# Performance work log

Hardware: AMD Instinct MI355X
Metric: run time of the kernel (lower is better)

## Reference

```python
import jax, jax.numpy as jnp
import numpy as np

D_MODEL = 1024
NHEAD = 16
HEAD_DIM = D_MODEL // NHEAD
EPS_NORM = 1e-6
EPS_RMS = 1e-6


def setup_inputs() -> dict:
    key = jax.random.key(0)
    ks = jax.random.split(key, 8)
    B, S = 2, 1024
    scale = 1.0 / np.sqrt(D_MODEL)
    x = jax.random.normal(ks[0], (B, S, D_MODEL), dtype=jnp.float32)
    Wq = jax.random.normal(ks[1], (D_MODEL, D_MODEL), dtype=jnp.float32) * scale
    Wk = jax.random.normal(ks[2], (D_MODEL, D_MODEL), dtype=jnp.float32) * scale
    Wv = jax.random.normal(ks[3], (D_MODEL, D_MODEL), dtype=jnp.float32) * scale
    Wb = jax.random.normal(ks[4], (NHEAD, D_MODEL), dtype=jnp.float32) * scale
    Wo = jax.random.normal(ks[5], (D_MODEL, D_MODEL), dtype=jnp.float32) * scale
    rms_w = jnp.ones((D_MODEL,), dtype=jnp.float32)
    return {"x": x, "Wq": Wq, "Wk": Wk, "Wv": Wv, "Wb": Wb, "Wo": Wo, "rms_w": rms_w}


def _l2_normalize(t):
    return t / (jnp.linalg.norm(t, axis=-1, keepdims=True) + EPS_NORM)


def _delta_forward(x, Wq, Wk, Wv, Wb, Wo, rms_w):
    B, S, dm = x.shape
    H, D = NHEAD, HEAD_DIM
    q = _l2_normalize(jax.nn.silu(x @ Wq.T).reshape(B, S, H, D))
    k = _l2_normalize(jax.nn.silu(x @ Wk.T).reshape(B, S, H, D))
    v = jax.nn.silu(x @ Wv.T).reshape(B, S, H, D)
    beta = jax.nn.sigmoid(x @ Wb.T) * 2.0  # (B,S,H), allow_neg_eigval doubles

    # time-major for scan: (S,B,H,D) / (S,B,H)
    qT = q.transpose(1, 0, 2, 3)
    kT = k.transpose(1, 0, 2, 3)
    vT = v.transpose(1, 0, 2, 3)
    bT = beta.transpose(1, 0, 2)

    def step(M, inp):
        qt, kt, vt, bt = inp
        # read state BEFORE update (strictly causal)
        out_t = jnp.einsum('bnh,bnhd->bnd', qt, M)
        retrieved = jnp.einsum('bnhd,bnd->bnh', M, kt)
        delta = vt - retrieved
        M = M + bt[..., None, None] * jnp.einsum('bnh,bnd->bnhd', kt, delta)
        return M, out_t

    M0 = jnp.zeros((B, H, D, D), dtype=x.dtype)
    _, outs = jax.lax.scan(step, M0, (qT, kT, vT, bT))  # (S,B,H,D)
    out = outs.transpose(1, 0, 2, 3).reshape(B, S, dm)

    # RMSNorm
    rms = jnp.sqrt(jnp.mean(out * out, axis=-1, keepdims=True) + EPS_RMS)
    out = out / rms * rms_w
    # output projection (dropout is identity in eval)
    return out @ Wo.T


def reference(x, Wq, Wk, Wv, Wb, Wo, rms_w):
    return _delta_forward(x, Wq, Wk, Wv, Wb, Wo, rms_w)
```

## Files before the change

kernel.cpp:

```cpp
#include <hip/hip_runtime.h>
#include <math.h>

#define D_MODEL 1024
#define NHEAD 16
#define HEAD_DIM 64
#define BATCH 2
#define SEQ 1024
#define ROWS (BATCH * SEQ)
#define RD (ROWS * D_MODEL)
#define WSZ (D_MODEL * D_MODEL)
#define CHUNK 64
#define NCHUNK (SEQ / CHUNK)

typedef __attribute__((ext_vector_type(8))) short bf16x8;
typedef __attribute__((ext_vector_type(8))) _Float16 f16x8;
typedef __attribute__((ext_vector_type(8))) unsigned short ushort8;
typedef __attribute__((ext_vector_type(4))) unsigned short us4;
typedef __attribute__((ext_vector_type(4))) float f32x4;
typedef __attribute__((ext_vector_type(4))) unsigned int uint4v;
typedef unsigned short ushort;

__device__ __forceinline__ void load_lds_16u(const unsigned short* g, unsigned short* l) {
    __builtin_amdgcn_global_load_lds((const __attribute__((address_space(1))) void*)g,
                                     (__attribute__((address_space(3))) void*)l, 16, 0, 0);
}
__device__ __forceinline__ unsigned short f2bf(float x) {
    unsigned int u = __float_as_uint(x);
    unsigned int r = (u + 0x7FFFu + ((u >> 16) & 1u)) >> 16;
    return (unsigned short)r;
}
__device__ __forceinline__ float bf2f(unsigned short h) {
    return __uint_as_float(((unsigned int)h) << 16);
}
__device__ __forceinline__ unsigned short f2h(float x) {
    _Float16 h = (_Float16)x;
    return __builtin_bit_cast(unsigned short, h);
}
__device__ __forceinline__ float lane_bcast(float v, int lane) {
    return __uint_as_float(__builtin_amdgcn_readlane(__float_as_uint(v), lane));
}
#define SUBST 512
#define FBUF (8 * SUBST * 2)
__device__ __forceinline__ int fidx(int r, int k) {
    return ((r >> 4) * 2 + (k >> 5)) * SUBST + ((((k & 31) >> 3) << 4) + (r & 15)) * 8 + (k & 7);
}


__global__ __launch_bounds__(256) void split_kernel(const float* __restrict__ X,
                                                    unsigned short* __restrict__ H,
                                                    int n4) {
    int i = blockIdx.x * 256 + threadIdx.x;
    if (i >= n4) return;
    float4 v = ((const float4*)X)[i];
    us4 h;
    h.x = f2h(v.x); h.y = f2h(v.y); h.z = f2h(v.z); h.w = f2h(v.w);
    ((us4*)H)[i] = h;
}

__global__ __launch_bounds__(256) void split3_kernel(const float* __restrict__ W0,
                                                     const float* __restrict__ W1,
                                                     const float* __restrict__ W2,
                                                     unsigned short* __restrict__ H0,
                                                     unsigned short* __restrict__ H1,
                                                     unsigned short* __restrict__ H2) {
    const int n4 = WSZ / 4;
    int i = blockIdx.x * 256 + threadIdx.x;
    const int which = i / n4;
    const int j = i - which * n4;
    const float* X = (which == 0) ? W0 : (which == 1) ? W1 : W2;
    unsigned short* H = (which == 0) ? H0 : (which == 1) ? H1 : H2;
    float4 v = ((const float4*)X)[j];
    us4 h;
    h.x = f2h(v.x); h.y = f2h(v.y); h.z = f2h(v.z); h.w = f2h(v.w);
    ((us4*)H)[j] = h;
}

template <int ACT>
__device__ __forceinline__ void gemm_core_f16(const unsigned short* __restrict__ Ah,
                                              const unsigned short* __restrict__ Bh,
                                              float* __restrict__ C,
                                              int M, int N, int K,
                                              unsigned short* LA0, unsigned short* LB0) {
    const int t = threadIdx.x;
    const int wave = t >> 6, lane = t & 63;
    const int wm = wave >> 1, wn = wave & 1;
    const int m16 = lane & 15, kg = lane >> 4;
    const int row0 = blockIdx.y * 128, col0 = blockIdx.x * 64;

    f32x4 acc[4][2];
#pragma unroll
    for (int i = 0; i < 4; ++i)
#pragma unroll
        for (int j = 0; j < 2; ++j) acc[i][j] = (f32x4){0.f, 0.f, 0.f, 0.f};

    for (int k0 = 0; k0 < K; k0 += 32) {
#pragma unroll
        for (int ci = 0; ci < 3; ++ci) {
            const int c = wave * 3 + ci;
            const unsigned short* src;
            unsigned short* dst;
            int g16, rbase;
            if (c < 8) { src = Ah; dst = &LA0[c * 512];       g16 = c;     rbase = row0; }
            else       { src = Bh; dst = &LB0[(c - 8) * 512]; g16 = c - 8; rbase = col0; }
            const unsigned short* gp = src + (size_t)(rbase + g16 * 16 + m16) * K + k0 + kg * 8;
            load_lds_16u(gp, dst);
        }
        __syncthreads();

        f16x8 fah[4], fbh[2];
#pragma unroll
        for (int mt = 0; mt < 4; ++mt)
            fah[mt] = *(const f16x8*)&LA0[(wm * 4 + mt) * 512 + lane * 8];
#pragma unroll
        for (int nt = 0; nt < 2; ++nt)
            fbh[nt] = *(const f16x8*)&LB0[(wn * 2 + nt) * 512 + lane * 8];
#pragma unroll
        for (int mt = 0; mt < 4; ++mt)
#pragma unroll
            for (int nt = 0; nt < 2; ++nt)
                acc[mt][nt] = __builtin_amdgcn_mfma_f32_16x16x32_f16(fah[mt], fbh[nt], acc[mt][nt], 0, 0, 0);
        __syncthreads();
    }

#pragma unroll
    for (int mt = 0; mt < 4; ++mt)
#pragma unroll
        for (int nt = 0; nt < 2; ++nt) {
            const int rowb = row0 + wm * 64 + mt * 16 + kg * 4;
            const int col  = col0 + wn * 32 + nt * 16 + m16;
#pragma unroll
            for (int rg = 0; rg < 4; ++rg) {
                float v = acc[mt][nt][rg];
                if (ACT == 1) v = v / (1.f + expf(-v));
                C[(size_t)(rowb + rg) * N + col] = v;
            }
        }
}

template <int ACT>
__global__ __launch_bounds__(256) void gemm_f16s(const unsigned short* __restrict__ Ah,
                                                 const unsigned short* __restrict__ Bh,
                                                 float* __restrict__ C,
                                                 int M, int N, int K) {
    __shared__ unsigned short LA[8 * 512];
    __shared__ unsigned short LB[4 * 512];
    gemm_core_f16<ACT>(Ah, Bh, C, M, N, K, LA, LB);
}

__global__ __launch_bounds__(256) void gemm_qkv(const unsigned short* __restrict__ Ah,
                                                const unsigned short* __restrict__ Bqh,
                                                const unsigned short* __restrict__ Bkh,
                                                const unsigned short* __restrict__ Bvh,
                                                float* __restrict__ Cq,
                                                float* __restrict__ Ck,
                                                float* __restrict__ Cv) {
    __shared__ unsigned short LA[8 * 512];
    __shared__ unsigned short LB[4 * 512];
    const int z = blockIdx.z;
    const unsigned short* Bh = (z == 0) ? Bqh : (z == 1) ? Bkh : Bvh;
    float* C = (z == 0) ? Cq : (z == 1) ? Ck : Cv;
    gemm_core_f16<1>(Ah, Bh, C, ROWS, D_MODEL, D_MODEL, LA, LB);
}

#define LDST 40
template <int ACT>
__global__ __launch_bounds__(256) void gemm_mfma(const float* __restrict__ A,
                                                 const float* __restrict__ B,
                                                 float* __restrict__ C,
                                                 int M, int N, int K) {
    __shared__ unsigned short Ahi[128 * LDST], Alo[128 * LDST];
    __shared__ unsigned short Bhi[128 * LDST], Blo[128 * LDST];

    const int t = threadIdx.x;
    const int wave = t >> 6, lane = t & 63;
    const int wm = wave >> 1, wn = wave & 1;
    const int row0 = blockIdx.y * 128, col0 = blockIdx.x * 128;
    const int sr = t >> 1;
    const int sh = t & 1;
    const int m16 = lane & 15, kg = lane >> 4;

    f32x4 acc[4][4];
#pragma unroll
    for (int i = 0; i < 4; ++i)
#pragma unroll
        for (int j = 0; j < 4; ++j) acc[i][j] = (f32x4){0.f, 0.f, 0.f, 0.f};

    const float* ga = A + (size_t)(row0 + sr) * K + sh * 16;
    const float* gb = B + (size_t)(col0 + sr) * K + sh * 16;
    const int sbase = sr * LDST + sh * 16;

    for (int k0 = 0; k0 < K; k0 += 32) {
        float af[16], bf[16];
#pragma unroll
        for (int i = 0; i < 4; ++i) {
            float4 a4 = *(const float4*)(ga + k0 + i * 4);
            float4 b4 = *(const float4*)(gb + k0 + i * 4);
            af[i * 4 + 0] = a4.x; af[i * 4 + 1] = a4.y; af[i * 4 + 2] = a4.z; af[i * 4 + 3] = a4.w;
            bf[i * 4 + 0] = b4.x; bf[i * 4 + 1] = b4.y; bf[i * 4 + 2] = b4.z; bf[i * 4 + 3] = b4.w;
        }
        ushort8 ah0, ah1, al0, al1, bh0, bh1, bl0, bl1;
#pragma unroll
        for (int j = 0; j < 8; ++j) {
            unsigned short h = f2bf(af[j]);       ah0[j] = h; al0[j] = f2bf(af[j] - bf2f(h));
            h = f2bf(af[j + 8]);                  ah1[j] = h; al1[j] = f2bf(af[j + 8] - bf2f(h));
            h = f2bf(bf[j]);                      bh0[j] = h; bl0[j] = f2bf(bf[j] - bf2f(h));
            h = f2bf(bf[j + 8]);                  bh1[j] = h; bl1[j] = f2bf(bf[j + 8] - bf2f(h));
        }
        *(ushort8*)&Ahi[sbase] = ah0;  *(ushort8*)&Ahi[sbase + 8] = ah1;
        *(ushort8*)&Alo[sbase] = al0;  *(ushort8*)&Alo[sbase + 8] = al1;
        *(ushort8*)&Bhi[sbase] = bh0;  *(ushort8*)&Bhi[sbase + 8] = bh1;
        *(ushort8*)&Blo[sbase] = bl0;  *(ushort8*)&Blo[sbase + 8] = bl1;
        __syncthreads();

        bf16x8 fah[4], fal[4], fbh[4], fbl[4];
#pragma unroll
        for (int i = 0; i < 4; ++i) {
            const int ar = (wm * 64 + i * 16 + m16) * LDST + kg * 8;
            const int br = (wn * 64 + i * 16 + m16) * LDST + kg * 8;
            fah[i] = *(const bf16x8*)&Ahi[ar];
            fal[i] = *(const bf16x8*)&Alo[ar];
            fbh[i] = *(const bf16x8*)&Bhi[br];
            fbl[i] = *(const bf16x8*)&Blo[br];
        }
#pragma unroll
        for (int i = 0; i < 4; ++i)
#pragma unroll
            for (int j = 0; j < 4; ++j) {
                acc[i][j] = __builtin_amdgcn_mfma_f32_16x16x32_bf16(fal[i], fbh[j], acc[i][j], 0, 0, 0);
                acc[i][j] = __builtin_amdgcn_mfma_f32_16x16x32_bf16(fah[i], fbl[j], acc[i][j], 0, 0, 0);
                acc[i][j] = __builtin_amdgcn_mfma_f32_16x16x32_bf16(fah[i], fbh[j], acc[i][j], 0, 0, 0);
            }
        __syncthreads();
    }

#pragma unroll
    for (int i = 0; i < 4; ++i)
#pragma unroll
        for (int j = 0; j < 4; ++j) {
            const int col = col0 + wn * 64 + j * 16 + m16;
            const int rowb = row0 + wm * 64 + i * 16 + kg * 4;
#pragma unroll
            for (int rg = 0; rg < 4; ++rg) {
                float v = acc[i][j][rg];
                if (ACT == 1) v = v / (1.f + expf(-v));
                C[(size_t)(rowb + rg) * N + col] = v;
            }
        }
}

__global__ __launch_bounds__(256) void beta_kernel(const float* __restrict__ x,
                                                   const float* __restrict__ Wb,
                                                   float* __restrict__ beta) {
    const int wave = blockIdx.x * 4 + (threadIdx.x >> 6);
    const int lane = threadIdx.x & 63;
    const float* xr = x + (size_t)wave * D_MODEL;
    float xv[16];
#pragma unroll
    for (int j = 0; j < 16; ++j) xv[j] = xr[lane + 64 * j];
    for (int n = 0; n < NHEAD; ++n) {
        const float* wr = Wb + (size_t)n * D_MODEL;
        float s = 0.f;
#pragma unroll
        for (int j = 0; j < 16; ++j) s += xv[j] * wr[lane + 64 * j];
#pragma unroll
        for (int off = 32; off; off >>= 1) s += __shfl_xor(s, off);
        if (lane == 0) beta[(size_t)wave * NHEAD + n] = 2.f / (1.f + expf(-s));
    }
}

__global__ __launch_bounds__(256) void norm_qk(float* __restrict__ Q,
                                               float* __restrict__ Kp) {
    const int TOT = ROWS * NHEAD;
    int wave = blockIdx.x * 4 + (threadIdx.x >> 6);
    const int lane = threadIdx.x & 63;
    float* T = (wave < TOT) ? Q : Kp;
    int w = (wave < TOT) ? wave : wave - TOT;
    float* p = T + (size_t)(w >> 4) * D_MODEL + (size_t)(w & 15) * HEAD_DIM;
    float v = p[lane];
    float ss = v * v;
#pragma unroll
    for (int off = 32; off; off >>= 1) ss += __shfl_xor(ss, off);
    p[lane] = v / (sqrtf(ss) + 1e-6f);
}

#define SMEM_SCAN 156160

__global__ __launch_bounds__(512, 1) void scan_chunked(const float* __restrict__ Qg,
                                                       const float* __restrict__ Kg,
                                                       const float* __restrict__ Vg,
                                                       const float* __restrict__ Btg,
                                                       float* __restrict__ Yg) {
    extern __shared__ char smem[];
    ushort* Mh_  = (ushort*)(smem + 0 * FBUF);
    ushort* Ml_  = (ushort*)(smem + 1 * FBUF);
    ushort* MTh_ = (ushort*)(smem + 2 * FBUF);
    ushort* MTl_ = (ushort*)(smem + 3 * FBUF);
    ushort* KTh_ = (ushort*)(smem + 4 * FBUF);
    ushort* KTl_ = (ushort*)(smem + 5 * FBUF);
    ushort* V0h_ = (ushort*)(smem + 6 * FBUF);
    ushort* V0l_ = (ushort*)(smem + 7 * FBUF);
    ushort* Wh_  = V0h_;
    ushort* Wl_  = V0l_;
    ushort* Gh_  = (ushort*)(smem + 8 * FBUF);
    ushort* Gl_  = (ushort*)(smem + 9 * FBUF);
    ushort* Kh_  = (ushort*)(smem + 10 * FBUF);
    ushort* Kl_  = (ushort*)(smem + 11 * FBUF);
    ushort* DTh_ = Kh_;
    ushort* DTl_ = Kl_;
    ushort* Qh_  = (ushort*)(smem + 12 * FBUF);
    ushort* Ql_  = (ushort*)(smem + 13 * FBUF);
    float*  C032 = (float*)(smem + 14 * FBUF);
    ushort* Ah_  = (ushort*)(smem + 14 * FBUF + 16640);
    ushort* Al_  = (ushort*)(smem + 15 * FBUF + 16640);
    float*  N32  = (float*)(smem + 16 * FBUF + 16640);
    float*  bAll = (float*)(smem + 16 * FBUF + 16640 + 4352);

    const int b = blockIdx.x >> 4;
    const int n = blockIdx.x & 15;
    const int t = threadIdx.x;
    const int wave = t >> 6, lane = t & 63;
    const int wm = wave >> 1, wn = wave & 1;
    const int m16 = lane & 15, kg = lane >> 4;
    const int bS = b * SEQ;
    const int nOff = n * HEAD_DIM;
    const int r = t >> 3, g = t & 7;

    f32x4 Macc[2];
    Macc[0] = (f32x4){0.f, 0.f, 0.f, 0.f};
    Macc[1] = (f32x4){0.f, 0.f, 0.f, 0.f};

    auto load_af = [&](const ushort* Xh, const ushort* Xl, int tm, bf16x8* oh, bf16x8* ol) {
        const int lo8 = lane * 8;
#pragma unroll
        for (int half = 0; half < 2; ++half) {
            oh[half] = *(const bf16x8*)&Xh[(tm * 2 + half) * SUBST + lo8];
            ol[half] = *(const bf16x8*)&Xl[(tm * 2 + half) * SUBST + lo8];
        }
    };
    auto prod_cA = [&](const bf16x8* ah, const bf16x8* al,
                       const ushort* Bh, const ushort* Bl, int tn, f32x4* acc) {
        const int lo8 = lane * 8;
#pragma unroll
        for (int half = 0; half < 2; ++half) {
#pragma unroll
            for (int j = 0; j < 2; ++j) {
                const int jg = tn * 2 + j;
                bf16x8 bh = *(const bf16x8*)&Bh[(jg * 2 + half) * SUBST + lo8];
                bf16x8 bl = *(const bf16x8*)&Bl[(jg * 2 + half) * SUBST + lo8];
                acc[j] = __builtin_amdgcn_mfma_f32_16x16x32_bf16(al[half], bh, acc[j], 0, 0, 0);
                acc[j] = __builtin_amdgcn_mfma_f32_16x16x32_bf16(ah[half], bl, acc[j], 0, 0, 0);
                acc[j] = __builtin_amdgcn_mfma_f32_16x16x32_bf16(ah[half], bh, acc[j], 0, 0, 0);
            }
        }
    };

    for (int i = t; i < SEQ; i += 512) bAll[i] = Btg[(size_t)(bS + i) * NHEAD + n];

    float4 pk0, pk1, pq0, pq1;
    float pv[8];
    auto issue_pf = [&](int cc) {
        const int so = cc * CHUNK;
        const float* gK = Kg + (size_t)(bS + so + r) * D_MODEL + nOff + g * 8;
        const float* gQ = Qg + (size_t)(bS + so + r) * D_MODEL + nOff + g * 8;
        pk0 = ((const float4*)gK)[0]; pk1 = ((const float4*)gK)[1];
        pq0 = ((const float4*)gQ)[0]; pq1 = ((const float4*)gQ)[1];
        const float* gV = Vg + (size_t)(bS + so) * D_MODEL + nOff;
#pragma unroll
        for (int j = 0; j < 2; ++j)
#pragma unroll
            for (int rg = 0; rg < 4; ++rg)
                pv[j * 4 + rg] = gV[(size_t)(wm * 16 + kg * 4 + rg) * D_MODEL + wn * 32 + j * 16 + m16];
    };
    issue_pf(0);

    for (int c = 0; c < NCHUNK; ++c) {
        const int s0 = c * CHUNK;

        {
            float kf[8] = {pk0.x, pk0.y, pk0.z, pk0.w, pk1.x, pk1.y, pk1.z, pk1.w};
            float qf[8] = {pq0.x, pq0.y, pq0.z, pq0.w, pq1.x, pq1.y, pq1.z, pq1.w};
            ushort8 kh8, kl8, qh8, ql8;
            ushort khv[8], klv[8];
#pragma unroll
            for (int e = 0; e < 8; ++e) {
                ushort h = f2bf(kf[e]);
                ushort l = f2bf(kf[e] - bf2f(h));
                khv[e] = h; klv[e] = l;
                kh8[e] = h; kl8[e] = l;
                h = f2bf(qf[e]); l = f2bf(qf[e] - bf2f(h));
                qh8[e] = h; ql8[e] = l;
            }
            const int o0 = fidx(r, g * 8);
            *(ushort8*)&Kh_[o0] = kh8;
            *(ushort8*)&Kl_[o0] = kl8;
            *(ushort8*)&Qh_[o0] = qh8;
            *(ushort8*)&Ql_[o0] = ql8;
#pragma unroll
            for (int e = 0; e < 8; ++e) {
                const int ib = fidx(g * 8 + e, r);
                KTh_[ib] = khv[e]; KTl_[ib] = klv[e];
            }
        }
        __syncthreads();

        bf16x8 kah[2], kal[2];
        f32x4 V0acc[2];
        {
            load_af(Kh_, Kl_, wm, kah, kal);
            V0acc[0] = (f32x4){0.f, 0.f, 0.f, 0.f};
            V0acc[1] = (f32x4){0.f, 0.f, 0.f, 0.f};
            if (c > 0) prod_cA(kah, kal, Mh_, Ml_, wn, V0acc);
#pragma unroll
            for (int j = 0; j < 2; ++j)
#pragma unroll
                for (int rg = 0; rg < 4; ++rg)
                    V0acc[j][rg] = pv[j * 4 + rg] - V0acc[j][rg];
#pragma unroll
            for (int j = 0; j < 2; ++j)
#pragma unroll
                for (int rg = 0; rg < 4; ++rg) {
                    const int row = wm * 16 + kg * 4 + rg, col = wn * 32 + j * 16 + m16;
                    const float v0 = V0acc[j][rg];
                    const ushort h = f2bf(v0);
                    const int ii = fidx(row, col);
                    V0h_[ii] = h; V0l_[ii] = f2bf(v0 - bf2f(h));
                }
            f32x4 aacc[2];
            aacc[0] = (f32x4){0.f, 0.f, 0.f, 0.f};
            aacc[1] = (f32x4){0.f, 0.f, 0.f, 0.f};
            prod_cA(kah, kal, Kh_, Kl_, wn, aacc);
#pragma unroll
            for (int j = 0; j < 2; ++j)
#pragma unroll
                for (int rg = 0; rg < 4; ++rg) {
                    const int row = wm * 16 + kg * 4 + rg, col = wn * 32 + j * 16 + m16;
                    const float av = aacc[j][rg];
                    const ushort h = f2bf(av);
                    const int ii = fidx(row, col);
                    Ah_[ii] = h; Al_[ii] = f2bf(av - bf2f(h));
                }
        }
        __syncthreads();

        {
            f32x4 cacc[2];
            cacc[0] = (f32x4){0.f, 0.f, 0.f, 0.f};
            cacc[1] = (f32x4){0.f, 0.f, 0.f, 0.f};
            prod_cA(kah, kal, V0h_, V0l_, wn, cacc);
#pragma unroll
            for (int j = 0; j < 2; ++j)
#pragma unroll
                for (int rg = 0; rg < 4; ++rg) {
                    const int row = wm * 16 + kg * 4 + rg, col = wn * 32 + j * 16 + m16;
                    C032[row * 65 + col] = cacc[j][rg];
                }
        }
        __syncthreads();

        if (c + 1 < NCHUNK) issue_pf(c + 1);

        f32x4 yacc[2][2];

        if (wave == 0) {
#pragma unroll
            for (int i0 = 0; i0 < 16; ++i0)
                ((uint4v*)Wh_)[i0 * 64 + lane] = (uint4v){0u, 0u, 0u, 0u};

#pragma unroll
            for (int J = 0; J < 4; ++J) {
                float Nreg[16];
                if (J > 0) {
                    const int lo8 = lane * 8;
#pragma unroll
                    for (int band = 0; band < 4; ++band) {
                        f32x4 acc1 = (f32x4){0.f, 0.f, 0.f, 0.f};
#pragma unroll
                        for (int half = 0; half < 2; ++half) {
                            bf16x8 ah = *(const bf16x8*)&Ah_[(band * 2 + half) * SUBST + lo8];
                            bf16x8 al = *(const bf16x8*)&Al_[(band * 2 + half) * SUBST + lo8];
                            bf16x8 bh = *(const bf16x8*)&Wh_[(J * 2 + half) * SUBST + lo8];
                            bf16x8 bl = *(const bf16x8*)&Wl_[(J * 2 + half) * SUBST + lo8];
                            acc1 = __builtin_amdgcn_mfma_f32_16x16x32_bf16(al, bh, acc1, 0, 0, 0);
                            acc1 = __builtin_amdgcn_mfma_f32_16x16x32_bf16(ah, bl, acc1, 0, 0, 0);
                            acc1 = __builtin_amdgcn_mfma_f32_16x16x32_bf16(ah, bh, acc1, 0, 0, 0);
                        }
#pragma unroll
                        for (int rg = 0; rg < 4; ++rg)
                            N32[(band * 16 + kg * 4 + rg) * 17 + m16] = acc1[rg];
                    }
#pragma unroll
                    for (int j = 0; j < 16; ++j) Nreg[j] = N32[lane * 17 + j];
                }

                float Areg[16], CNreg[16];
                {
                    bf16x8 a0 = *(const bf16x8*)&Ah_[fidx(lane, 16 * J)];
                    bf16x8 a1 = *(const bf16x8*)&Ah_[fidx(lane, 16 * J + 8)];
                    bf16x8 b0 = *(const bf16x8*)&Al_[fidx(lane, 16 * J)];
                    bf16x8 b1 = *(const bf16x8*)&Al_[fidx(lane, 16 * J + 8)];
#pragma unroll
                    for (int e = 0; e < 8; ++e) {
                        Areg[e]     = bf2f((ushort)a0[e]) + bf2f((ushort)b0[e]);
                        Areg[e + 8] = bf2f((ushort)a1[e]) + bf2f((ushort)b1[e]);
                    }
#pragma unroll
                    for (int j = 0; j < 16; ++j) CNreg[j] = C032[lane * 65 + 16 * J + j];
                    if (J > 0) {
#pragma unroll
                        for (int j = 0; j < 16; ++j) CNreg[j] += Nreg[j];
                    }
                }
                float bvreg = bAll[s0 + 16 * J + m16];

                float wreg[16];
#pragma unroll
                for (int j = 0; j < 16; ++j) {
                    float sA = CNreg[j], sB = 0.f;
#pragma unroll
                    for (int jj = 0; jj < 16; ++jj) {
                        if (jj < j) {
                            float pr = Areg[jj] * lane_bcast(wreg[jj], 16 * J + j);
                            if (jj & 1) sB += pr; else sA += pr;
                        }
                    }
                    float sum = sA + sB;
                    float beta_s = lane_bcast(bvreg, j);
                    wreg[j] = (lane > 16 * J + j) ? (-beta_s * sum) : 0.f;
                }

                {
                    ushort8 h8[2], l8[2];
#pragma unroll
                    for (int e = 0; e < 16; ++e) {
                        ushort h = f2bf(wreg[e]);
                        h8[e >> 3][e & 7] = h;
                        l8[e >> 3][e & 7] = f2bf(wreg[e] - bf2f(h));
                    }
                    const int o0 = fidx(lane, 16 * J), o1 = fidx(lane, 16 * J + 8);
                    *(ushort8*)&Wh_[o0] = h8[0]; *(ushort8*)&Wh_[o1] = h8[1];
                    *(ushort8*)&Wl_[o0] = l8[0]; *(ushort8*)&Wl_[o1] = l8[1];
                }
            }
        } else {
            const int nt_w = (wave == 4) ? 0 : ((wave <= 2) ? 2 : 1);
            const int wi = (wave < 4) ? (wave - 1) : (wave - 2);
#pragma unroll
            for (int ti = 0; ti < 2; ++ti) {
                if (ti >= nt_w) continue;
                const int T = (ti == 0) ? wi : (wi + 6);
                const int twm = T >> 1, twn = T & 1;
                bf16x8 qh2[2], ql2[2];
                load_af(Qh_, Ql_, twm, qh2, ql2);
                yacc[ti][0] = (f32x4){0.f, 0.f, 0.f, 0.f};
                yacc[ti][1] = (f32x4){0.f, 0.f, 0.f, 0.f};
                if (c > 0) prod_cA(qh2, ql2, MTh_, MTl_, twn, yacc[ti]);
                const bool gz = (twm * 16 + 15) <= (twn * 32);
                f32x4 ga[2];
                ga[0] = (f32x4){0.f, 0.f, 0.f, 0.f};
                ga[1] = (f32x4){0.f, 0.f, 0.f, 0.f};
                if (!gz) prod_cA(qh2, ql2, Kh_, Kl_, twn, ga);
#pragma unroll
                for (int j = 0; j < 2; ++j)
#pragma unroll
                    for (int rg = 0; rg < 4; ++rg) {
                        const int row = twm * 16 + kg * 4 + rg, col = twn * 32 + j * 16 + m16;
                        const float gv = (row > col) ? ga[j][rg] : 0.f;
                        const ushort h = f2bf(gv);
                        const int ii = fidx(row, col);
                        Gh_[ii] = h; Gl_[ii] = f2bf(gv - bf2f(h));
                    }
            }
        }
        __syncthreads();

        {
            f32x4 dacc[2];
            dacc[0] = V0acc[0]; dacc[1] = V0acc[1];
            bf16x8 wh2[2], wl2[2];
            load_af(Wh_, Wl_, wm, wh2, wl2);
            prod_cA(wh2, wl2, KTh_, KTl_, wn, dacc);
#pragma unroll
            for (int j = 0; j < 2; ++j)
#pragma unroll
                for (int rg = 0; rg < 4; ++rg) {
                    const int row = wm * 16 + kg * 4 + rg, col = wn * 32 + j * 16 + m16;
                    const float dv = dacc[j][rg] * bAll[s0 + row];
                    const ushort h = f2bf(dv);
                    const int ii = fidx(col, row);
                    DTh_[ii] = h; DTl_[ii] = f2bf(dv - bf2f(h));
                }
        }
        __syncthreads();

        if (wave != 0) {
            const int nt_w = (wave == 4) ? 0 : ((wave <= 2) ? 2 : 1);
            const int wi = (wave < 4) ? (wave - 1) : (wave - 2);
#pragma unroll
            for (int ti = 0; ti < 2; ++ti) {
                if (ti >= nt_w) continue;
                const int T = (ti == 0) ? wi : (wi + 6);
                const int twm = T >> 1, twn = T & 1;
                bf16x8 gh2[2], gl2[2];
                load_af(Gh_, Gl_, twm, gh2, gl2);
                prod_cA(gh2, gl2, DTh_, DTl_, twn, yacc[ti]);
#pragma unroll
                for (int j = 0; j < 2; ++j)
#pragma unroll
                    for (int rg = 0; rg < 4; ++rg) {
                        const int row = twm * 16 + kg * 4 + rg, col = twn * 32 + j * 16 + m16;
                        Yg[(size_t)(bS + s0 + row) * D_MODEL + nOff + col] = yacc[ti][j][rg];
                    }
            }
        }
        {
            bf16x8 kth[2], ktl[2];
            load_af(KTh_, KTl_, wm, kth, ktl);
            prod_cA(kth, ktl, DTh_, DTl_, wn, Macc);
            if (c < NCHUNK - 1) {
#pragma unroll
                for (int j = 0; j < 2; ++j)
#pragma unroll
                    for (int rg = 0; rg < 4; ++rg) {
                        const int row = wm * 16 + kg * 4 + rg, col = wn * 32 + j * 16 + m16;
                        const float mv = Macc[j][rg];
                        const ushort h = f2bf(mv), l = f2bf(mv - bf2f(h));
                        const int ii = fidx(row, col);
                        Mh_[ii] = h; Ml_[ii] = l;
                        const int iT = fidx(col, row);
                        MTh_[iT] = h; MTl_[iT] = l;
                    }
            }
        }
        __syncthreads();
    }
}

template <int SPLIT>
__global__ __launch_bounds__(256) void rmsnorm_kernel(float* __restrict__ Y,
                                                      const float* __restrict__ w,
                                                      unsigned short* __restrict__ H) {
    __shared__ float red[4];
    float* y = Y + (size_t)blockIdx.x * D_MODEL;
    const int t = threadIdx.x;
    const int wv = t >> 6, ln = t & 63;
    float4 v = ((float4*)y)[t];
    float ss = v.x * v.x + v.y * v.y + v.z * v.z + v.w * v.w;
#pragma unroll
    for (int off = 32; off; off >>= 1) ss += __shfl_xor(ss, off);
    if (ln == 0) red[wv] = ss;
    __syncthreads();
    float tot = red[0] + red[1] + red[2] + red[3];
    float inv = 1.f / sqrtf(tot * (1.f / D_MODEL) + 1e-6f);
    const float4 wv4 = ((const float4*)w)[t];
    v.x *= inv * wv4.x; v.y *= inv * wv4.y;
    v.z *= inv * wv4.z; v.w *= inv * wv4.w;
    if (SPLIT) {
        us4 h;
        h.x = f2h(v.x); h.y = f2h(v.y); h.z = f2h(v.z); h.w = f2h(v.w);
        size_t i = (size_t)blockIdx.x * 256 + t;
        ((us4*)H)[i] = h;
    } else {
        ((float4*)y)[t] = v;
    }
}

extern "C" void kernel_launch(void* const* d_in, const int* in_sizes, int n_in,
                              void* d_out, int out_size, void* d_ws, size_t ws_size,
                              hipStream_t stream) {
    const float* x     = (const float*)d_in[0];
    const float* Wq    = (const float*)d_in[1];
    const float* Wk    = (const float*)d_in[2];
    const float* Wv    = (const float*)d_in[3];
    const float* Wb    = (const float*)d_in[4];
    const float* Wo    = (const float*)d_in[5];
    const float* rms_w = (const float*)d_in[6];
    float* out = (float*)d_out;

    char* p = (char*)d_ws;
    float* Q  = (float*)p;  p += (size_t)RD * 4;
    float* Kp = (float*)p;  p += (size_t)RD * 4;
    float* Vp = (float*)p;  p += (size_t)RD * 4;
    float* Y  = (float*)p;  p += (size_t)RD * 4;
    float* Bt = (float*)p;  p += (size_t)32768 * 4;
    unsigned short* xh  = (unsigned short*)p;  p += (size_t)RD * 2;
    unsigned short* xl  = (unsigned short*)p;  p += (size_t)RD * 2;
    unsigned short* Wsh = (unsigned short*)p;  p += (size_t)WSZ * 2;
    unsigned short* Wsl = (unsigned short*)p;  p += (size_t)WSZ * 2;
    const size_t need_fast = (size_t)RD * 16 + 131072 + (size_t)RD * 4 + (size_t)WSZ * 4;
    const bool fast = ws_size >= need_fast;

    unsigned short* Wkh = (unsigned short*)Y;
    unsigned short* Wvh = Wkh + WSZ;

    (void)hipFuncSetAttribute(reinterpret_cast<const void*>(scan_chunked),
                              hipFuncAttributeMaxDynamicSharedMemorySize, SMEM_SCAN);

    if (fast) {
        dim3 ggrid(D_MODEL / 64, ROWS / 128);
        dim3 qgrid(D_MODEL / 64, ROWS / 128, 3);
        split_kernel<<<RD / 4 / 256, 256, 0, stream>>>(x, xh, RD / 4);
        split3_kernel<<<3 * WSZ / 4 / 256, 256, 0, stream>>>(Wq, Wk, Wv, Wsh, Wkh, Wvh);
        gemm_qkv<<<qgrid, 256, 0, stream>>>(xh, Wsh, Wkh, Wvh, Q, Kp, Vp);
        beta_kernel<<<ROWS / 4, 256, 0, stream>>>(x, Wb, Bt);
        norm_qk<<<2 * ROWS * NHEAD / 4, 256, 0, stream>>>(Q, Kp);
        scan_chunked<<<BATCH * NHEAD, 512, SMEM_SCAN, stream>>>(Q, Kp, Vp, Bt, Y);
        rmsnorm_kernel<1><<<ROWS, 256, 0, stream>>>(Y, rms_w, xh);
        split_kernel<<<WSZ / 4 / 256, 256, 0, stream>>>(Wo, Wsh, WSZ / 4);
        gemm_f16s<0><<<ggrid, 256, 0, stream>>>(xh, Wsh, out, ROWS, D_MODEL, D_MODEL);
    } else {
        dim3 ggrid(D_MODEL / 128, ROWS / 128);
        gemm_mfma<1><<<ggrid, 256, 0, stream>>>(x, Wq, Q, ROWS, D_MODEL, D_MODEL);
        gemm_mfma<1><<<ggrid, 256, 0, stream>>>(x, Wk, Kp, ROWS, D_MODEL, D_MODEL);
        gemm_mfma<1><<<ggrid, 256, 0, stream>>>(x, Wv, Vp, ROWS, D_MODEL, D_MODEL);
        beta_kernel<<<ROWS / 4, 256, 0, stream>>>(x, Wb, Bt);
        norm_qk<<<2 * ROWS * NHEAD / 4, 256, 0, stream>>>(Q, Kp);
        scan_chunked<<<BATCH * NHEAD, 512, SMEM_SCAN, stream>>>(Q, Kp, Vp, Bt, Y);
        rmsnorm_kernel<0><<<ROWS, 256, 0, stream>>>(Y, rms_w, nullptr);
        gemm_mfma<0><<<ggrid, 256, 0, stream>>>(Y, Wo, out, ROWS, D_MODEL, D_MODEL);
    }
}
```

Before: 387.3 us.

## Fuse q/k L2 normalization into QKV GEMM epilogue and batch Wo conversion

Moves the per-head L2 normalization of q and k into the QKV GEMM epilogue. Each 64-column block tile covers exactly one head, so row sums of squares are reduced with lane shuffles plus a small shared-memory exchange between the two column waves. This removes the separate norm_qk kernel and its extra read and write of Q and K. It also folds the Wo fp16 conversion into the same launch as Wq/Wk/Wv, dropping one more kernel launch. In exchange the GEMM epilogue gains an extra barrier and some register pressure from holding all activated outputs.

```diff
diff --git a/kernel.cpp b/kernel.cpp
--- a/kernel.cpp
+++ b/kernel.cpp
@@ -57,18 +57,20 @@
     ((us4*)H)[i] = h;
 }
 
-__global__ __launch_bounds__(256) void split3_kernel(const float* __restrict__ W0,
+__global__ __launch_bounds__(256) void split4_kernel(const float* __restrict__ W0,
                                                      const float* __restrict__ W1,
                                                      const float* __restrict__ W2,
+                                                     const float* __restrict__ W3,
                                                      unsigned short* __restrict__ H0,
                                                      unsigned short* __restrict__ H1,
-                                                     unsigned short* __restrict__ H2) {
+                                                     unsigned short* __restrict__ H2,
+                                                     unsigned short* __restrict__ H3) {
     const int n4 = WSZ / 4;
     int i = blockIdx.x * 256 + threadIdx.x;
     const int which = i / n4;
     const int j = i - which * n4;
-    const float* X = (which == 0) ? W0 : (which == 1) ? W1 : W2;
-    unsigned short* H = (which == 0) ? H0 : (which == 1) ? H1 : H2;
+    const float* X = (which == 0) ? W0 : (which == 1) ? W1 : (which == 2) ? W2 : W3;
+    unsigned short* H = (which == 0) ? H0 : (which == 1) ? H1 : (which == 2) ? H2 : H3;
     float4 v = ((const float4*)X)[j];
     us4 h;
     h.x = f2h(v.x); h.y = f2h(v.y); h.z = f2h(v.z); h.w = f2h(v.w);
@@ -80,7 +82,8 @@
                                               const unsigned short* __restrict__ Bh,
                                               float* __restrict__ C,
                                               int M, int N, int K,
-                                              unsigned short* LA0, unsigned short* LB0) {
+                                              unsigned short* LA0, unsigned short* LB0,
+                                              float* NP, bool do_norm) {
     const int t = threadIdx.x;
     const int wave = t >> 6, lane = t & 63;
     const int wm = wave >> 1, wn = wave & 1;
@@ -122,6 +125,38 @@
         __syncthreads();
     }
 
+    float sv[4][2][4];
+#pragma unroll
+    for (int mt = 0; mt < 4; ++mt)
+#pragma unroll
+        for (int nt = 0; nt < 2; ++nt)
+#pragma unroll
+            for (int rg = 0; rg < 4; ++rg) {
+                float v = acc[mt][nt][rg];
+                if (ACT == 1) v = v / (1.f + expf(-v));
+                sv[mt][nt][rg] = v;
+            }
+    if (do_norm) {
+#pragma unroll
+        for (int mt = 0; mt < 4; ++mt)
+#pragma unroll
+            for (int rg = 0; rg < 4; ++rg) {
+                float ss = sv[mt][0][rg] * sv[mt][0][rg] + sv[mt][1][rg] * sv[mt][1][rg];
+#pragma unroll
+                for (int off = 8; off; off >>= 1) ss += __shfl_xor(ss, off);
+                if (m16 == 0) NP[wn * 128 + wm * 64 + mt * 16 + kg * 4 + rg] = ss;
+            }
+        __syncthreads();
+#pragma unroll
+        for (int mt = 0; mt < 4; ++mt)
+#pragma unroll
+            for (int rg = 0; rg < 4; ++rg) {
+                const int rw = wm * 64 + mt * 16 + kg * 4 + rg;
+                const float inv = 1.f / (sqrtf(NP[rw] + NP[128 + rw]) + 1e-6f);
+                sv[mt][0][rg] *= inv;
+                sv[mt][1][rg] *= inv;
+            }
+    }
 #pragma unroll
     for (int mt = 0; mt < 4; ++mt)
 #pragma unroll
@@ -129,11 +164,8 @@
             const int rowb = row0 + wm * 64 + mt * 16 + kg * 4;
             const int col  = col0 + wn * 32 + nt * 16 + m16;
 #pragma unroll
-            for (int rg = 0; rg < 4; ++rg) {
-                float v = acc[mt][nt][rg];
-                if (ACT == 1) v = v / (1.f + expf(-v));
-                C[(size_t)(rowb + rg) * N + col] = v;
-            }
+            for (int rg = 0; rg < 4; ++rg)
+                C[(size_t)(rowb + rg) * N + col] = sv[mt][nt][rg];
         }
 }
 
@@ -144,7 +176,7 @@
                                                  int M, int N, int K) {
     __shared__ unsigned short LA[8 * 512];
     __shared__ unsigned short LB[4 * 512];
-    gemm_core_f16<ACT>(Ah, Bh, C, M, N, K, LA, LB);
+    gemm_core_f16<ACT>(Ah, Bh, C, M, N, K, LA, LB, nullptr, false);
 }
 
 __global__ __launch_bounds__(256) void gemm_qkv(const unsigned short* __restrict__ Ah,
@@ -156,10 +188,11 @@
                                                 float* __restrict__ Cv) {
     __shared__ unsigned short LA[8 * 512];
     __shared__ unsigned short LB[4 * 512];
+    __shared__ float NP[2 * 128];
     const int z = blockIdx.z;
     const unsigned short* Bh = (z == 0) ? Bqh : (z == 1) ? Bkh : Bvh;
     float* C = (z == 0) ? Cq : (z == 1) ? Ck : Cv;
-    gemm_core_f16<1>(Ah, Bh, C, ROWS, D_MODEL, D_MODEL, LA, LB);
+    gemm_core_f16<1>(Ah, Bh, C, ROWS, D_MODEL, D_MODEL, LA, LB, NP, z < 2);
 }
 
 #define LDST 40
@@ -691,6 +724,7 @@
 
     unsigned short* Wkh = (unsigned short*)Y;
     unsigned short* Wvh = Wkh + WSZ;
+    unsigned short* Woh = Wsl;
 
     (void)hipFuncSetAttribute(reinterpret_cast<const void*>(scan_chunked),
                               hipFuncAttributeMaxDynamicSharedMemorySize, SMEM_SCAN);
@@ -699,14 +733,13 @@
         dim3 ggrid(D_MODEL / 64, ROWS / 128);
         dim3 qgrid(D_MODEL / 64, ROWS / 128, 3);
         split_kernel<<<RD / 4 / 256, 256, 0, stream>>>(x, xh, RD / 4);
-        split3_kernel<<<3 * WSZ / 4 / 256, 256, 0, stream>>>(Wq, Wk, Wv, Wsh, Wkh, Wvh);
+        split4_kernel<<<WSZ / 256, 256, 0, stream>>>(Wq, Wk, Wv, Wo,
+                                                     Wsh, Wkh, Wvh, Woh);
         gemm_qkv<<<qgrid, 256, 0, stream>>>(xh, Wsh, Wkh, Wvh, Q, Kp, Vp);
         beta_kernel<<<ROWS / 4, 256, 0, stream>>>(x, Wb, Bt);
-        norm_qk<<<2 * ROWS * NHEAD / 4, 256, 0, stream>>>(Q, Kp);
         scan_chunked<<<BATCH * NHEAD, 512, SMEM_SCAN, stream>>>(Q, Kp, Vp, Bt, Y);
         rmsnorm_kernel<1><<<ROWS, 256, 0, stream>>>(Y, rms_w, xh);
-        split_kernel<<<WSZ / 4 / 256, 256, 0, stream>>>(Wo, Wsh, WSZ / 4);
-        gemm_f16s<0><<<ggrid, 256, 0, stream>>>(xh, Wsh, out, ROWS, D_MODEL, D_MODEL);
+        gemm_f16s<0><<<ggrid, 256, 0, stream>>>(xh, Woh, out, ROWS, D_MODEL, D_MODEL);
     } else {
         dim3 ggrid(D_MODEL / 128, ROWS / 128);
         gemm_mfma<1><<<ggrid, 256, 0, stream>>>(x, Wq, Q, ROWS, D_MODEL, D_MODEL);
```

New measurement: 376.7 us, median of 2. 2.7% less time.
